# Kernel optimization log

Measured on AMD Instinct MI355X. Metric: run time of the kernel, lower is better.

Reference implementation:

```python
import jax, jax.numpy as jnp
import numpy as np

N = 100000   # nodes
E = 1600000  # edges
IN = 128     # input feature dim
HID = 64     # hidden = IN // 2
OUT = 8      # output_size
B = 16384    # lookup batch


def sage_conv(x, src, dst, W_l, W_r, b, n):
    # PyG SAGEConv (aggr='mean', root_weight=True):
    # out = lin_l(mean_{j in N(i)} x_j) + lin_r(x_i)
    msgs = x[src]                                              # [E, F] gather
    agg = jax.ops.segment_sum(msgs, dst, num_segments=n)       # [N, F] scatter-add
    deg = jax.ops.segment_sum(jnp.ones((src.shape[0],), x.dtype), dst, num_segments=n)
    mean = agg / jnp.maximum(deg, 1.0)[:, None]                # zero-degree -> 0
    return mean @ W_l + x @ W_r + b


def setup_inputs() -> dict:
    key = jax.random.key(0)
    ks = jax.random.split(key, 10)
    node_feats = jax.random.normal(ks[0], (N, IN), dtype=jnp.float32)
    edge_index = jax.random.randint(ks[1], (2, E), 0, N, dtype=jnp.int64)
    idx = jax.random.randint(ks[2], (B,), 0, N, dtype=jnp.int64)
    dropout_mask = jax.random.uniform(ks[3], (N, HID), dtype=jnp.float32)
    s1 = 1.0 / np.sqrt(IN)
    s2 = 1.0 / np.sqrt(HID)
    W1_l = jax.random.normal(ks[4], (IN, HID), dtype=jnp.float32) * s1
    W1_r = jax.random.normal(ks[5], (IN, HID), dtype=jnp.float32) * s1
    b1 = jnp.zeros((HID,), dtype=jnp.float32)
    W2_l = jax.random.normal(ks[6], (HID, OUT), dtype=jnp.float32) * s2
    W2_r = jax.random.normal(ks[7], (HID, OUT), dtype=jnp.float32) * s2
    b2 = jnp.zeros((OUT,), dtype=jnp.float32)
    return {"node_feats": node_feats, "edge_index": edge_index, "idx": idx,
            "dropout_mask": dropout_mask, "W1_l": W1_l, "W1_r": W1_r, "b1": b1,
            "W2_l": W2_l, "W2_r": W2_r, "b2": b2}


def reference(node_feats, edge_index, idx, dropout_mask, W1_l, W1_r, b1, W2_l, W2_r, b2):
    n = node_feats.shape[0]
    src, dst = edge_index[0], edge_index[1]
    h = sage_conv(node_feats, src, dst, W1_l, W1_r, b1, n)     # [N, HID]
    h = jax.nn.relu(h)
    keep = (dropout_mask > 0.5).astype(h.dtype)                # F.dropout p=0.5
    h = h * keep * 2.0                                         # inverted dropout scale 1/(1-p)
    emb = sage_conv(h, src, dst, W2_l, W2_r, b2, n)            # [N, OUT]
    return emb[idx]                                            # [B, OUT]
```

## Files before the change

kernel.cpp:

```cpp
#include <hip/hip_runtime.h>
#include <hip/hip_fp16.h>

#define IN_F 128
#define HID_F 64
#define OUT_F 8

#define BSHIFT 7
#define BGRAN 128
#define BCAP 2688
#define NBUK_MAX 784
#define CHUNK 2048
#define EPT (CHUNK / 256)
#define CEPT ((BCAP + 255) / 256)

typedef _Float16 f16x8 __attribute__((ext_vector_type(8)));
typedef float f32x4 __attribute__((ext_vector_type(4)));

__global__ __launch_bounds__(256) void prep(
    const float* __restrict__ Wl, const float* __restrict__ Wr,
    _Float16* __restrict__ Wt, int* __restrict__ bcur, int nbuk) {
  int blk = blockIdx.x;
  if (blk < 16) {
    int i = blk * 256 + threadIdx.x;
    int n = i & 127;
    int k4 = (i >> 7) * 4;
    _Float16 hv[4];
#pragma unroll
    for (int j = 0; j < 4; ++j) {
      float v = (n < HID_F) ? Wl[(k4 + j) * HID_F + n]
                            : Wr[(k4 + j) * HID_F + (n - HID_F)];
      hv[j] = (_Float16)v;
    }
    *(uint2*)(Wt + (size_t)n * IN_F + k4) = *(uint2*)hv;
  } else {
    for (int i = threadIdx.x; i < nbuk; i += 256) bcur[i] = i * BCAP;
  }
}

__global__ __launch_bounds__(256) void bucket_scatter(
    const int* __restrict__ src, const int* __restrict__ dst,
    int* __restrict__ bcur, int* __restrict__ ebuf, int n_edges) {
  __shared__ int hist[NBUK_MAX];
  __shared__ int base[NBUK_MAX];
  int t = threadIdx.x;
  for (int i = t; i < NBUK_MAX; i += 256) hist[i] = 0;
  __syncthreads();
  int e0 = blockIdx.x * CHUNK;
  int pk[EPT];
  int bk[EPT];
  int rk[EPT];
#pragma unroll
  for (int k = 0; k < EPT; ++k) {
    int e = e0 + k * 256 + t;
    if (e < n_edges) {
      int s = src[e];
      int d = dst[e];
      bk[k] = d >> BSHIFT;
      pk[k] = ((d & (BGRAN - 1)) << 24) | s;
      rk[k] = atomicAdd(&hist[bk[k]], 1);
    } else {
      bk[k] = -1;
    }
  }
  __syncthreads();
  for (int i = t; i < NBUK_MAX; i += 256) {
    int c = hist[i];
    base[i] = c ? atomicAdd(&bcur[i], c) : 0;
  }
  __syncthreads();
#pragma unroll
  for (int k = 0; k < EPT; ++k) {
    if (bk[k] >= 0) ebuf[base[bk[k]] + rk[k]] = pk[k];
  }
}

__global__ __launch_bounds__(256) void bucket_csr(
    const int* __restrict__ ebuf, const int* __restrict__ bcur,
    uint2* __restrict__ nd, int* __restrict__ csr_src, int n_nodes) {
  __shared__ int hist[BGRAN];
  __shared__ int excl_s[BGRAN];
  __shared__ int lds_src[BCAP];
  int b = blockIdx.x;
  int t = threadIdx.x;
  if (t < BGRAN) hist[t] = 0;
  __syncthreads();
  int beg = b * BCAP;
  int cnt = bcur[b] - beg;
  int pk[CEPT];
  int rk[CEPT];
#pragma unroll
  for (int u = 0; u < CEPT; ++u) {
    int j = t + u * 256;
    if (j < cnt) {
      pk[u] = ebuf[beg + j];
      rk[u] = atomicAdd(&hist[(unsigned)pk[u] >> 24], 1);
    } else {
      pk[u] = -1;
    }
  }
  __syncthreads();
  if (t < 64) {
    int h0 = hist[2 * t];
    int h1 = hist[2 * t + 1];
    int ps = h0 + h1;
#pragma unroll
    for (int dd = 1; dd < 64; dd <<= 1) {
      int u = __shfl_up(ps, dd);
      if (t >= dd) ps += u;
    }
    excl_s[2 * t] = ps - h1 - h0;
    excl_s[2 * t + 1] = ps - h1;
  }
  __syncthreads();
  if (t < BGRAN) {
    int node = b * BGRAN + t;
    if (node < n_nodes)
      nd[node] = make_uint2((unsigned)(beg + excl_s[t]), (unsigned)hist[t]);
  }
#pragma unroll
  for (int u = 0; u < CEPT; ++u) {
    if (pk[u] != -1) {
      int bin = (unsigned)pk[u] >> 24;
      lds_src[excl_s[bin] + rk[u]] = pk[u] & 0xFFFFFF;
    }
  }
  __syncthreads();
  for (int j = t; j < cnt; j += 256) csr_src[beg + j] = lds_src[j];
}

#define K1_ROWS 64
#define XSH 136
__global__ __launch_bounds__(256) void k1_proj(
    const float* __restrict__ x,
    const _Float16* __restrict__ Wt,
    const float* __restrict__ b1,
    const float* __restrict__ mask,
    __half* __restrict__ y1h,
    __half* __restrict__ r1h,
    unsigned long long* __restrict__ mbits,
    int n_nodes) {
  __shared__ _Float16 XS[K1_ROWS * XSH];
  int tid = threadIdx.x;
  int w = tid >> 6;
  int lane = tid & 63;
  int n0 = blockIdx.x * K1_ROWS;
  int m = lane & 15;
  int quad = lane >> 4;

  float mv[16];
#pragma unroll
  for (int u = 0; u < 16; ++u) {
    int node = n0 + w * 16 + u;
    mv[u] = (node < n_nodes) ? mask[(size_t)node * HID_F + lane] : 0.f;
  }

  f16x8 af[2][4];
#pragma unroll
  for (int ti = 0; ti < 2; ++ti) {
    int t = w + ti * 4;
#pragma unroll
    for (int kk = 0; kk < 4; ++kk)
      af[ti][kk] = *(const f16x8*)(Wt + (size_t)(t * 16 + m) * IN_F + kk * 32 + quad * 8);
  }
  float4 b1v = *(const float4*)(b1 + w * 16 + quad * 4);

#pragma unroll
  for (int p = 0; p < 8; ++p) {
    int i = tid + p * 256;
    int row = i >> 5;
    int k4 = (i & 31) * 4;
    int gs = min(n0 + row, n_nodes - 1);
    float4 v = *(const float4*)(x + (size_t)gs * IN_F + k4);
    _Float16 hv[4] = {(_Float16)v.x, (_Float16)v.y, (_Float16)v.z, (_Float16)v.w};
    *(uint2*)&XS[row * XSH + k4] = *(uint2*)hv;
  }
  __syncthreads();

#pragma unroll
  for (int rt = 0; rt < 4; ++rt) {
    f32x4 acc0 = f32x4{0.f, 0.f, 0.f, 0.f};
    f32x4 acc1 = f32x4{0.f, 0.f, 0.f, 0.f};
#pragma unroll
    for (int kk = 0; kk < 4; ++kk) {
      f16x8 bx = *(const f16x8*)&XS[(rt * 16 + m) * XSH + kk * 32 + quad * 8];
      acc0 = __builtin_amdgcn_mfma_f32_16x16x32_f16(af[0][kk], bx, acc0, 0, 0, 0);
      acc1 = __builtin_amdgcn_mfma_f32_16x16x32_f16(af[1][kk], bx, acc1, 0, 0, 0);
    }
    int node = n0 + rt * 16 + m;
    if (node < n_nodes) {
      __half hy[4], hr[4];
#pragma unroll
      for (int r = 0; r < 4; ++r) {
        hy[r] = __float2half(acc0[r]);
        hr[r] = __float2half(acc1[r] + ((const float*)&b1v)[r]);
      }
      *(uint2*)(y1h + (size_t)node * HID_F + w * 16 + quad * 4) = *(uint2*)hy;
      *(uint2*)(r1h + (size_t)node * HID_F + w * 16 + quad * 4) = *(uint2*)hr;
    }
  }

#pragma unroll
  for (int u = 0; u < 16; ++u) {
    int node = n0 + w * 16 + u;
    unsigned long long bb = __ballot(mv[u] > 0.5f);
    if (lane == 0 && node < n_nodes) mbits[node] = bb;
  }
}

__global__ __launch_bounds__(256) void agg1_fused(
    const __half* __restrict__ y1h,
    const __half* __restrict__ r1h,
    const uint2* __restrict__ nd,
    const int* __restrict__ csr_src,
    const unsigned long long* __restrict__ mbits,
    __half* __restrict__ h_h,
    int n_nodes, int npw) {
  int wid = (blockIdx.x * 256 + threadIdx.x) >> 6;
  int lane = threadIdx.x & 63;
  int q = lane >> 4;
  int f4 = lane & 15;
  int n0 = wid * npw;
  if (n0 >= n_nodes) return;
  int nend = min(n0 + npw, n_nodes);
  const char* yb = (const char*)y1h;
  unsigned foff = (unsigned)(f4 * 8);

#define ACCB(g0, g1, g2, g3)                                 \
  {                                                          \
    __half2 hx = *(const __half2*)&(g0).x;                   \
    __half2 hy = *(const __half2*)&(g0).y;                   \
    hx = __hadd2(hx, *(const __half2*)&(g1).x);              \
    hy = __hadd2(hy, *(const __half2*)&(g1).y);              \
    hx = __hadd2(hx, *(const __half2*)&(g2).x);              \
    hy = __hadd2(hy, *(const __half2*)&(g2).y);              \
    hx = __hadd2(hx, *(const __half2*)&(g3).x);              \
    hy = __hadd2(hy, *(const __half2*)&(g3).y);              \
    float2 fx = __half22float2(hx);                          \
    float2 fy = __half22float2(hy);                          \
    a0 += fx.x; a1 += fx.y; a2 += fy.x; a3 += fy.y;          \
  }

  uint2 be_c = nd[__builtin_amdgcn_readfirstlane(n0)];
  unsigned pidx[4] = {0u, 0u, 0u, 0u};
  {
    int d0 = (int)be_c.y;
    if (d0 > 0) {
      const int* cp0 = csr_src + (int)be_c.x;
      int dm = d0 - 1;
#pragma unroll
      for (int k = 0; k < 4; ++k)
        pidx[k] = (unsigned)cp0[min(4 * k + q, dm)];
    }
  }

  for (int n = n0; n < nend; ++n) {
    int nu = __builtin_amdgcn_readfirstlane(n);
    unsigned long long mb = mbits[nu];
    size_t o = (size_t)nu * HID_F + f4 * 4;
    uint2 rg = *(const uint2*)(r1h + o);
    uint2 be_n = make_uint2(0u, 0u);
    if (n + 1 < nend) {
      int nun = __builtin_amdgcn_readfirstlane(n + 1);
      be_n = nd[nun];
    }

    int d = (int)be_c.y;
    const int* cp = csr_src + (int)be_c.x;
    float a0 = 0.f, a1 = 0.f, a2 = 0.f, a3 = 0.f;

    if (d > 0) {
      uint2 g0 = *(const uint2*)(yb + ((pidx[0] << 7) + foff));
      uint2 g1 = *(const uint2*)(yb + ((pidx[1] << 7) + foff));
      uint2 g2 = *(const uint2*)(yb + ((pidx[2] << 7) + foff));
      uint2 g3 = *(const uint2*)(yb + ((pidx[3] << 7) + foff));
      uint2 zz = make_uint2(0u, 0u);
      if (q >= d) g0 = zz;
      if (4 + q >= d) g1 = zz;
      if (8 + q >= d) g2 = zz;
      if (12 + q >= d) g3 = zz;
      ACCB(g0, g1, g2, g3)
    }
    int j = 16;
    for (; j + 16 <= d; j += 16) {
      unsigned s0 = (unsigned)cp[j + q];
      unsigned s1 = (unsigned)cp[j + 4 + q];
      unsigned s2 = (unsigned)cp[j + 8 + q];
      unsigned s3 = (unsigned)cp[j + 12 + q];
      uint2 g0 = *(const uint2*)(yb + ((s0 << 7) + foff));
      uint2 g1 = *(const uint2*)(yb + ((s1 << 7) + foff));
      uint2 g2 = *(const uint2*)(yb + ((s2 << 7) + foff));
      uint2 g3 = *(const uint2*)(yb + ((s3 << 7) + foff));
      ACCB(g0, g1, g2, g3)
    }
    if (j < d) {
      int dm = d - 1;
      int e0 = j + q, e1 = j + 4 + q, e2 = j + 8 + q, e3 = j + 12 + q;
      unsigned s0 = (unsigned)cp[min(e0, dm)];
      unsigned s1 = (unsigned)cp[min(e1, dm)];
      unsigned s2 = (unsigned)cp[min(e2, dm)];
      unsigned s3 = (unsigned)cp[min(e3, dm)];
      uint2 g0 = *(const uint2*)(yb + ((s0 << 7) + foff));
      uint2 g1 = *(const uint2*)(yb + ((s1 << 7) + foff));
      uint2 g2 = *(const uint2*)(yb + ((s2 << 7) + foff));
      uint2 g3 = *(const uint2*)(yb + ((s3 << 7) + foff));
      uint2 zz = make_uint2(0u, 0u);
      if (e0 >= d) g0 = zz;
      if (e1 >= d) g1 = zz;
      if (e2 >= d) g2 = zz;
      if (e3 >= d) g3 = zz;
      ACCB(g0, g1, g2, g3)
    }

    if (n + 1 < nend) {
      int dn = (int)be_n.y;
      if (dn > 0) {
        const int* cpn = csr_src + (int)be_n.x;
        int dmn = dn - 1;
#pragma unroll
        for (int k = 0; k < 4; ++k)
          pidx[k] = (unsigned)cpn[min(4 * k + q, dmn)];
      }
    }

    a0 += __shfl_xor(a0, 16); a0 += __shfl_xor(a0, 32);
    a1 += __shfl_xor(a1, 16); a1 += __shfl_xor(a1, 32);
    a2 += __shfl_xor(a2, 16); a2 += __shfl_xor(a2, 32);
    a3 += __shfl_xor(a3, 16); a3 += __shfl_xor(a3, 32);
    if (q == 0) {
      float inv = 1.0f / fmaxf((float)d, 1.0f);
      float2 r01 = __half22float2(*(const __half2*)&rg.x);
      float2 r23 = __half22float2(*(const __half2*)&rg.y);
      float vx = fmaxf(a0 * inv + r01.x, 0.f);
      float vy = fmaxf(a1 * inv + r01.y, 0.f);
      float vz = fmaxf(a2 * inv + r23.x, 0.f);
      float vw = fmaxf(a3 * inv + r23.y, 0.f);
      int fb = f4 * 4;
      vx = ((mb >> (fb + 0)) & 1ull) ? vx * 2.f : 0.f;
      vy = ((mb >> (fb + 1)) & 1ull) ? vy * 2.f : 0.f;
      vz = ((mb >> (fb + 2)) & 1ull) ? vz * 2.f : 0.f;
      vw = ((mb >> (fb + 3)) & 1ull) ? vw * 2.f : 0.f;
      __half hh[4] = {__float2half(vx), __float2half(vy),
                      __float2half(vz), __float2half(vw)};
      *(uint2*)(h_h + o) = *(uint2*)hh;
    }
    be_c = be_n;
  }
#undef ACCB
}

__global__ __launch_bounds__(256) void k3b_z(
    const __half* __restrict__ h_h,
    const float* __restrict__ W2l,
    __half* __restrict__ z,
    int n_nodes) {
  __shared__ float WS[HID_F][OUT_F];
  int tid = threadIdx.x;
  if (tid < 128) {
    float4 w = *(const float4*)(W2l + tid * 4);
    *(float4*)&WS[tid >> 1][(tid & 1) * 4] = w;
  }
  __syncthreads();
  int node = blockIdx.x * blockDim.x + tid;
  if (node >= n_nodes) return;
  const __half* hr = h_h + (size_t)node * HID_F;
  float acc[8] = {0, 0, 0, 0, 0, 0, 0, 0};
  for (int k = 0; k < HID_F; k += 8) {
    uint4 hv = *(const uint4*)(hr + k);
    float2 f0 = __half22float2(*(const __half2*)&hv.x);
    float2 f1 = __half22float2(*(const __half2*)&hv.y);
    float2 f2 = __half22float2(*(const __half2*)&hv.z);
    float2 f3 = __half22float2(*(const __half2*)&hv.w);
    float hh[8] = {f0.x, f0.y, f1.x, f1.y, f2.x, f2.y, f3.x, f3.y};
#pragma unroll
    for (int j = 0; j < 8; ++j) {
      float4 w0 = *(const float4*)&WS[k + j][0];
      float4 w1 = *(const float4*)&WS[k + j][4];
      acc[0] += hh[j] * w0.x; acc[1] += hh[j] * w0.y;
      acc[2] += hh[j] * w0.z; acc[3] += hh[j] * w0.w;
      acc[4] += hh[j] * w1.x; acc[5] += hh[j] * w1.y;
      acc[6] += hh[j] * w1.z; acc[7] += hh[j] * w1.w;
    }
  }
  __half hz[8];
#pragma unroll
  for (int j = 0; j < 8; ++j) hz[j] = __float2half(acc[j]);
  *(uint4*)(z + (size_t)node * OUT_F) = *(uint4*)hz;
}

__global__ __launch_bounds__(256) void out_fused(
    const int* __restrict__ idx,
    const __half* __restrict__ z,
    const uint2* __restrict__ nd,
    const int* __restrict__ csr_src,
    const __half* __restrict__ h_h,
    const float* __restrict__ W2r,
    const float* __restrict__ b2,
    float* __restrict__ out,
    int n_batch) {
  int b = (blockIdx.x * blockDim.x + threadIdx.x) >> 6;
  int lane = threadIdx.x & 63;
  if (b >= n_batch) return;
  int bu = __builtin_amdgcn_readfirstlane(b);
  int i = idx[bu];
  int iu = __builtin_amdgcn_readfirstlane(i);
  int e8 = lane >> 3;
  int o = lane & 7;
  uint2 be = nd[iu];
  uint4 hv = *(const uint4*)(h_h + (size_t)iu * HID_F + e8 * 8);
  int beg = (int)be.x;
  int d = (int)be.y;
  const int* cp = csr_src + beg;
  const char* zb = (const char*)z;
  unsigned ooff = (unsigned)(o * 2);
  float acc = 0.f;
  int j = e8;
  for (; j + 8 < d; j += 16) {
    unsigned s0 = (unsigned)cp[j];
    unsigned s1 = (unsigned)cp[j + 8];
    float z0 = __half2float(*(const __half*)(zb + ((s0 << 4) + ooff)));
    float z1 = __half2float(*(const __half*)(zb + ((s1 << 4) + ooff)));
    acc += z0 + z1;
  }
  if (j < d) {
    unsigned s0 = (unsigned)cp[j];
    acc += __half2float(*(const __half*)(zb + ((s0 << 4) + ooff)));
  }
  float dv = fmaxf((float)d, 1.0f);
  float v = acc / dv;
  float2 f0 = __half22float2(*(const __half2*)&hv.x);
  float2 f1 = __half22float2(*(const __half2*)&hv.y);
  float2 f2 = __half22float2(*(const __half2*)&hv.z);
  float2 f3 = __half22float2(*(const __half2*)&hv.w);
  float hh[8] = {f0.x, f0.y, f1.x, f1.y, f2.x, f2.y, f3.x, f3.y};
#pragma unroll
  for (int jj = 0; jj < 8; ++jj) {
    int k = e8 * 8 + jj;
    v += hh[jj] * W2r[k * OUT_F + o];
  }
  v += __shfl_xor(v, 8);
  v += __shfl_xor(v, 16);
  v += __shfl_xor(v, 32);
  if (e8 == 0) out[(size_t)b * OUT_F + o] = v + b2[o];
}

extern "C" void kernel_launch(void* const* d_in, const int* in_sizes, int n_in,
                              void* d_out, int out_size, void* d_ws, size_t ws_size,
                              hipStream_t stream) {
  const float* x    = (const float*)d_in[0];
  const int*   ei   = (const int*)d_in[1];
  const int*   idx  = (const int*)d_in[2];
  const float* mask = (const float*)d_in[3];
  const float* W1l  = (const float*)d_in[4];
  const float* W1r  = (const float*)d_in[5];
  const float* b1   = (const float*)d_in[6];
  const float* W2l  = (const float*)d_in[7];
  const float* W2r  = (const float*)d_in[8];
  const float* b2   = (const float*)d_in[9];
  float* out = (float*)d_out;

  int n_nodes = in_sizes[0] / IN_F;
  int n_edges = in_sizes[1] / 2;
  int n_batch = in_sizes[2];
  const int* src = ei;
  const int* dst = ei + n_edges;

  int nbuk = (n_nodes + BGRAN - 1) / BGRAN;
  int nchunk = (n_edges + CHUNK - 1) / CHUNK;

  char* ws = (char*)d_ws;
  size_t off = 0;
  __half* y1h = (__half*)(ws + off); off += (size_t)n_nodes * HID_F * 2;
  __half* r1h = (__half*)(ws + off); off += (size_t)n_nodes * HID_F * 2;
  __half* h_h = (__half*)(ws + off); off += (size_t)n_nodes * HID_F * 2;
  __half* z   = (__half*)(ws + off); off += (size_t)n_nodes * OUT_F * 2;
  unsigned long long* mbits = (unsigned long long*)(ws + off); off += (size_t)n_nodes * 8;
  _Float16* Wt = (_Float16*)(ws + off); off += (size_t)IN_F * IN_F * 2;
  int* ebuf    = (int*)(ws + off); off += (size_t)nbuk * BCAP * 4;
  int* csr_src = (int*)(ws + off); off += (size_t)nbuk * BCAP * 4;
  uint2* nd    = (uint2*)(ws + off); off += (size_t)n_nodes * 8;
  int* bcur    = (int*)(ws + off); off += NBUK_MAX * 4;

  prep<<<17, 256, 0, stream>>>(W1l, W1r, Wt, bcur, nbuk);
  bucket_scatter<<<nchunk, 256, 0, stream>>>(src, dst, bcur, ebuf, n_edges);
  k1_proj<<<(n_nodes + K1_ROWS - 1) / K1_ROWS, 256, 0, stream>>>(
      x, Wt, b1, mask, y1h, r1h, mbits, n_nodes);
  bucket_csr<<<nbuk, 256, 0, stream>>>(ebuf, bcur, nd, csr_src, n_nodes);

  {
    int tw = 8192;
    int npw = (n_nodes + tw - 1) / tw;
    int nw = (n_nodes + npw - 1) / npw;
    int blocks = (nw + 3) / 4;
    agg1_fused<<<blocks, 256, 0, stream>>>(
        y1h, r1h, nd, csr_src, mbits, h_h, n_nodes, npw);
  }

  k3b_z<<<(n_nodes + 255) / 256, 256, 0, stream>>>(h_h, W2l, z, n_nodes);
  {
    long long th = (long long)n_batch * 64;
    out_fused<<<(int)((th + 255) / 256), 256, 0, stream>>>(
        idx, z, nd, csr_src, h_h, W2r, b2, out, n_batch);
  }
}
```

Baseline: 237.3 us.

## Merge edge bucket scatter and layer-1 projection into one heterogeneous launch

Fuses the bucket_scatter and k1_proj kernels into a single build1 launch where the first nchunk blocks do edge bucketing and the rest do the MFMA projection. The two independent phases can then run concurrently on the GPU, and one launch boundary and tail drain go away. Both phases share one LDS buffer sized for the projection tile. The mask loads now happen after the __syncthreads rather than before it. The k3b_z launch gets a no-op `0 ? 0 : 256` expression.

```diff
diff --git a/kernel.cpp b/kernel.cpp
--- a/kernel.cpp
+++ b/kernel.cpp
@@ -12,6 +12,9 @@
 #define CHUNK 2048
 #define EPT (CHUNK / 256)
 #define CEPT ((BCAP + 255) / 256)
+
+#define K1_ROWS 64
+#define XSH 136
 
 typedef _Float16 f16x8 __attribute__((ext_vector_type(8)));
 typedef float f32x4 __attribute__((ext_vector_type(4)));
@@ -37,40 +40,115 @@
   }
 }
 
-__global__ __launch_bounds__(256) void bucket_scatter(
+__global__ __launch_bounds__(256) void build1(
     const int* __restrict__ src, const int* __restrict__ dst,
-    int* __restrict__ bcur, int* __restrict__ ebuf, int n_edges) {
-  __shared__ int hist[NBUK_MAX];
-  __shared__ int base[NBUK_MAX];
+    int* __restrict__ bcur, int* __restrict__ ebuf, int n_edges,
+    const float* __restrict__ x, const _Float16* __restrict__ Wt,
+    const float* __restrict__ b1, const float* __restrict__ mask,
+    __half* __restrict__ y1h, __half* __restrict__ r1h,
+    unsigned long long* __restrict__ mbits, int n_nodes, int nchunk) {
+  __shared__ __align__(16) char SMEM[K1_ROWS * XSH * 2];
   int t = threadIdx.x;
-  for (int i = t; i < NBUK_MAX; i += 256) hist[i] = 0;
+
+  if (blockIdx.x < nchunk) {
+    int* hist = (int*)SMEM;
+    int* base = (int*)(SMEM + NBUK_MAX * 4);
+    for (int i = t; i < NBUK_MAX; i += 256) hist[i] = 0;
+    __syncthreads();
+    int e0 = blockIdx.x * CHUNK;
+    int pk[EPT];
+    int bk[EPT];
+    int rk[EPT];
+#pragma unroll
+    for (int k = 0; k < EPT; ++k) {
+      int e = e0 + k * 256 + t;
+      if (e < n_edges) {
+        int s = src[e];
+        int d = dst[e];
+        bk[k] = d >> BSHIFT;
+        pk[k] = ((d & (BGRAN - 1)) << 24) | s;
+        rk[k] = atomicAdd(&hist[bk[k]], 1);
+      } else {
+        bk[k] = -1;
+      }
+    }
+    __syncthreads();
+    for (int i = t; i < NBUK_MAX; i += 256) {
+      int c = hist[i];
+      base[i] = c ? atomicAdd(&bcur[i], c) : 0;
+    }
+    __syncthreads();
+#pragma unroll
+    for (int k = 0; k < EPT; ++k) {
+      if (bk[k] >= 0) ebuf[base[bk[k]] + rk[k]] = pk[k];
+    }
+    return;
+  }
+
+  _Float16* XS = (_Float16*)SMEM;
+  int w = t >> 6;
+  int lane = t & 63;
+  int n0 = (blockIdx.x - nchunk) * K1_ROWS;
+  int m = lane & 15;
+  int quad = lane >> 4;
+
+  f16x8 af[2][4];
+#pragma unroll
+  for (int ti = 0; ti < 2; ++ti) {
+    int tt = w + ti * 4;
+#pragma unroll
+    for (int kk = 0; kk < 4; ++kk)
+      af[ti][kk] = *(const f16x8*)(Wt + (size_t)(tt * 16 + m) * IN_F + kk * 32 + quad * 8);
+  }
+  float4 b1v = *(const float4*)(b1 + w * 16 + quad * 4);
+
+#pragma unroll
+  for (int p = 0; p < 8; ++p) {
+    int i = t + p * 256;
+    int row = i >> 5;
+    int k4 = (i & 31) * 4;
+    int gs = min(n0 + row, n_nodes - 1);
+    float4 v = *(const float4*)(x + (size_t)gs * IN_F + k4);
+    _Float16 hv[4] = {(_Float16)v.x, (_Float16)v.y, (_Float16)v.z, (_Float16)v.w};
+    *(uint2*)&XS[row * XSH + k4] = *(uint2*)hv;
+  }
   __syncthreads();
-  int e0 = blockIdx.x * CHUNK;
-  int pk[EPT];
-  int bk[EPT];
-  int rk[EPT];
-#pragma unroll
-  for (int k = 0; k < EPT; ++k) {
-    int e = e0 + k * 256 + t;
-    if (e < n_edges) {
-      int s = src[e];
-      int d = dst[e];
-      bk[k] = d >> BSHIFT;
-      pk[k] = ((d & (BGRAN - 1)) << 24) | s;
-      rk[k] = atomicAdd(&hist[bk[k]], 1);
-    } else {
-      bk[k] = -1;
-    }
-  }
-  __syncthreads();
-  for (int i = t; i < NBUK_MAX; i += 256) {
-    int c = hist[i];
-    base[i] = c ? atomicAdd(&bcur[i], c) : 0;
-  }
-  __syncthreads();
-#pragma unroll
-  for (int k = 0; k < EPT; ++k) {
-    if (bk[k] >= 0) ebuf[base[bk[k]] + rk[k]] = pk[k];
+
+  float mv[16];
+#pragma unroll
+  for (int u = 0; u < 16; ++u) {
+    int node = n0 + w * 16 + u;
+    mv[u] = (node < n_nodes) ? mask[(size_t)node * HID_F + lane] : 0.f;
+  }
+
+#pragma unroll
+  for (int rt = 0; rt < 4; ++rt) {
+    f32x4 acc0 = f32x4{0.f, 0.f, 0.f, 0.f};
+    f32x4 acc1 = f32x4{0.f, 0.f, 0.f, 0.f};
+#pragma unroll
+    for (int kk = 0; kk < 4; ++kk) {
+      f16x8 bx = *(const f16x8*)&XS[(rt * 16 + m) * XSH + kk * 32 + quad * 8];
+      acc0 = __builtin_amdgcn_mfma_f32_16x16x32_f16(af[0][kk], bx, acc0, 0, 0, 0);
+      acc1 = __builtin_amdgcn_mfma_f32_16x16x32_f16(af[1][kk], bx, acc1, 0, 0, 0);
+    }
+    int node = n0 + rt * 16 + m;
+    if (node < n_nodes) {
+      __half hy[4], hr[4];
+#pragma unroll
+      for (int r = 0; r < 4; ++r) {
+        hy[r] = __float2half(acc0[r]);
+        hr[r] = __float2half(acc1[r] + ((const float*)&b1v)[r]);
+      }
+      *(uint2*)(y1h + (size_t)node * HID_F + w * 16 + quad * 4) = *(uint2*)hy;
+      *(uint2*)(r1h + (size_t)node * HID_F + w * 16 + quad * 4) = *(uint2*)hr;
+    }
+  }
+
+#pragma unroll
+  for (int u = 0; u < 16; ++u) {
+    int node = n0 + w * 16 + u;
+    unsigned long long bb = __ballot(mv[u] > 0.5f);
+    if (lane == 0 && node < n_nodes) mbits[node] = bb;
   }
 }
 
@@ -126,85 +204,6 @@
   }
   __syncthreads();
   for (int j = t; j < cnt; j += 256) csr_src[beg + j] = lds_src[j];
-}
-
-#define K1_ROWS 64
-#define XSH 136
-__global__ __launch_bounds__(256) void k1_proj(
-    const float* __restrict__ x,
-    const _Float16* __restrict__ Wt,
-    const float* __restrict__ b1,
-    const float* __restrict__ mask,
-    __half* __restrict__ y1h,
-    __half* __restrict__ r1h,
-    unsigned long long* __restrict__ mbits,
-    int n_nodes) {
-  __shared__ _Float16 XS[K1_ROWS * XSH];
-  int tid = threadIdx.x;
-  int w = tid >> 6;
-  int lane = tid & 63;
-  int n0 = blockIdx.x * K1_ROWS;
-  int m = lane & 15;
-  int quad = lane >> 4;
-
-  float mv[16];
-#pragma unroll
-  for (int u = 0; u < 16; ++u) {
-    int node = n0 + w * 16 + u;
-    mv[u] = (node < n_nodes) ? mask[(size_t)node * HID_F + lane] : 0.f;
-  }
-
-  f16x8 af[2][4];
-#pragma unroll
-  for (int ti = 0; ti < 2; ++ti) {
-    int t = w + ti * 4;
-#pragma unroll
-    for (int kk = 0; kk < 4; ++kk)
-      af[ti][kk] = *(const f16x8*)(Wt + (size_t)(t * 16 + m) * IN_F + kk * 32 + quad * 8);
-  }
-  float4 b1v = *(const float4*)(b1 + w * 16 + quad * 4);
-
-#pragma unroll
-  for (int p = 0; p < 8; ++p) {
-    int i = tid + p * 256;
-    int row = i >> 5;
-    int k4 = (i & 31) * 4;
-    int gs = min(n0 + row, n_nodes - 1);
-    float4 v = *(const float4*)(x + (size_t)gs * IN_F + k4);
-    _Float16 hv[4] = {(_Float16)v.x, (_Float16)v.y, (_Float16)v.z, (_Float16)v.w};
-    *(uint2*)&XS[row * XSH + k4] = *(uint2*)hv;
-  }
-  __syncthreads();
-
-#pragma unroll
-  for (int rt = 0; rt < 4; ++rt) {
-    f32x4 acc0 = f32x4{0.f, 0.f, 0.f, 0.f};
-    f32x4 acc1 = f32x4{0.f, 0.f, 0.f, 0.f};
-#pragma unroll
-    for (int kk = 0; kk < 4; ++kk) {
-      f16x8 bx = *(const f16x8*)&XS[(rt * 16 + m) * XSH + kk * 32 + quad * 8];
-      acc0 = __builtin_amdgcn_mfma_f32_16x16x32_f16(af[0][kk], bx, acc0, 0, 0, 0);
-      acc1 = __builtin_amdgcn_mfma_f32_16x16x32_f16(af[1][kk], bx, acc1, 0, 0, 0);
-    }
-    int node = n0 + rt * 16 + m;
-    if (node < n_nodes) {
-      __half hy[4], hr[4];
-#pragma unroll
-      for (int r = 0; r < 4; ++r) {
-        hy[r] = __float2half(acc0[r]);
-        hr[r] = __float2half(acc1[r] + ((const float*)&b1v)[r]);
-      }
-      *(uint2*)(y1h + (size_t)node * HID_F + w * 16 + quad * 4) = *(uint2*)hy;
-      *(uint2*)(r1h + (size_t)node * HID_F + w * 16 + quad * 4) = *(uint2*)hr;
-    }
-  }
-
-#pragma unroll
-  for (int u = 0; u < 16; ++u) {
-    int node = n0 + w * 16 + u;
-    unsigned long long bb = __ballot(mv[u] > 0.5f);
-    if (lane == 0 && node < n_nodes) mbits[node] = bb;
-  }
 }
 
 __global__ __launch_bounds__(256) void agg1_fused(
@@ -466,6 +465,7 @@
 
   int nbuk = (n_nodes + BGRAN - 1) / BGRAN;
   int nchunk = (n_edges + CHUNK - 1) / CHUNK;
+  int nk1 = (n_nodes + K1_ROWS - 1) / K1_ROWS;
 
   char* ws = (char*)d_ws;
   size_t off = 0;
@@ -481,9 +481,11 @@
   int* bcur    = (int*)(ws + off); off += NBUK_MAX * 4;
 
   prep<<<17, 256, 0, stream>>>(W1l, W1r, Wt, bcur, nbuk);
-  bucket_scatter<<<nchunk, 256, 0, stream>>>(src, dst, bcur, ebuf, n_edges);
-  k1_proj<<<(n_nodes + K1_ROWS - 1) / K1_ROWS, 256, 0, stream>>>(
-      x, Wt, b1, mask, y1h, r1h, mbits, n_nodes);
+
+  build1<<<nchunk + nk1, 256, 0, stream>>>(
+      src, dst, bcur, ebuf, n_edges,
+      x, Wt, b1, mask, y1h, r1h, mbits, n_nodes, nchunk);
+
   bucket_csr<<<nbuk, 256, 0, stream>>>(ebuf, bcur, nd, csr_src, n_nodes);
 
   {
@@ -495,7 +497,7 @@
         y1h, r1h, nd, csr_src, mbits, h_h, n_nodes, npw);
   }
 
-  k3b_z<<<(n_nodes + 255) / 256, 256, 0, stream>>>(h_h, W2l, z, n_nodes);
+  k3b_z<<<(n_nodes + 255) / 256, 0 ? 0 : 256, 0, stream>>>(h_h, W2l, z, n_nodes);
   {
     long long th = (long long)n_batch * 64;
     out_fused<<<(int)((th + 255) / 256), 256, 0, stream>>>(
```

Result: no change. 235.1 us (-0.9%).
